# Kernel tuning notes

Measured on AMD Instinct MI355X. Metric: run time of the kernel, lower is better.

The kernel has to match this reference:

```python
import jax, jax.numpy as jnp
import numpy as np

MODEL_DIM = 1024
N_HEADS = 16
HEAD_DIM = 64  # q_dim == k_dim == v_dim


def setup_inputs() -> dict:
    key = jax.random.key(0)
    ks = jax.random.split(key, 7)
    B, S = 4, 2048
    scale = 1.0 / np.sqrt(MODEL_DIM)
    return {
        "q": jax.random.normal(ks[0], (B, S, MODEL_DIM), dtype=jnp.float32),
        "k": jax.random.normal(ks[1], (B, S, MODEL_DIM), dtype=jnp.float32),
        "v": jax.random.normal(ks[2], (B, S, MODEL_DIM), dtype=jnp.float32),
        # Linear weights stored as [out, in] like torch; no biases.
        "wq": jax.random.normal(ks[3], (N_HEADS * HEAD_DIM, MODEL_DIM), dtype=jnp.float32) * scale,
        "wk": jax.random.normal(ks[4], (N_HEADS * HEAD_DIM, MODEL_DIM), dtype=jnp.float32) * scale,
        "wv": jax.random.normal(ks[5], (N_HEADS * HEAD_DIM, MODEL_DIM), dtype=jnp.float32) * scale,
        "wo": jax.random.normal(ks[6], (MODEL_DIM, N_HEADS * HEAD_DIM), dtype=jnp.float32) * scale,
    }


def reference(q, k, v, wq, wk, wv, wo):
    B, Sq, _ = q.shape
    Sk = k.shape[1]
    # projections: [B,S,D] @ W^T -> [B,S,H*dh] -> [B,H,S,dh]
    qh = (q @ wq.T).reshape(B, Sq, N_HEADS, HEAD_DIM).transpose(0, 2, 1, 3)
    kh = (k @ wk.T).reshape(B, Sk, N_HEADS, HEAD_DIM).transpose(0, 2, 1, 3)
    vh = (v @ wv.T).reshape(B, Sk, N_HEADS, HEAD_DIM).transpose(0, 2, 1, 3)
    # scores [B,H,Sq,Sk], scaled by sqrt(k_dim)
    scores = jnp.einsum('bhqd,bhkd->bhqk', qh, kh) / jnp.sqrt(jnp.float32(HEAD_DIM))
    attn = jax.nn.softmax(scores, axis=-1)
    ctx = jnp.einsum('bhqk,bhkd->bhqd', attn, vh)  # [B,H,Sq,dh]
    ctx = ctx.transpose(0, 2, 1, 3).reshape(B, Sq, N_HEADS * HEAD_DIM)
    return ctx @ wo.T
```

## Files before the change

### kernel.cpp

```cpp
#include <hip/hip_runtime.h>
#include <cstdint>
#include <cstddef>


typedef _Float16 f16x8 __attribute__((ext_vector_type(8)));
typedef _Float16 f16x4 __attribute__((ext_vector_type(4)));
typedef _Float16 f16x2 __attribute__((ext_vector_type(2)));
typedef __fp16 h16x2 __attribute__((ext_vector_type(2)));
typedef float f32x4 __attribute__((ext_vector_type(4)));
typedef float f32x16 __attribute__((ext_vector_type(16)));
typedef unsigned u32x4 __attribute__((ext_vector_type(4)));
typedef int i32x2 __attribute__((ext_vector_type(2)));

#define LDS_CAST(p) ((__attribute__((address_space(3))) void*)(p))
#define GLB_CAST(p) ((const __attribute__((address_space(1))) void*)(p))

__device__ __forceinline__ void gload_lds16(const void* g, void* l) {
  __builtin_amdgcn_global_load_lds(GLB_CAST(g), LDS_CAST(l), 16, 0, 0);
}

__device__ __forceinline__ float fexp2(float x) {
#if __has_builtin(__builtin_amdgcn_exp2f)
  return __builtin_amdgcn_exp2f(x);
#else
  return exp2f(x);
#endif
}

__device__ __forceinline__ f16x2 pkrtz(float a, float b) {
  h16x2 r = __builtin_amdgcn_cvt_pkrtz(a, b);
  return __builtin_bit_cast(f16x2, r);
}

__device__ __forceinline__ float dot2acc(f16x2 a, float acc) {
#if __has_builtin(__builtin_amdgcn_fdot2)
  const f16x2 one2 = {(_Float16)1.0f, (_Float16)1.0f};
  return __builtin_amdgcn_fdot2(a, one2, acc, false);
#else
  return acc + (float)a[0] + (float)a[1];
#endif
}

__device__ __forceinline__ void pl32swap(unsigned& a, unsigned& b) {
#if __has_builtin(__builtin_amdgcn_permlane32_swap)
  i32x2 r = __builtin_amdgcn_permlane32_swap((int)a, (int)b, false, false);
  a = (unsigned)r[0];
  b = (unsigned)r[1];
#else
  asm("v_permlane32_swap_b32 %0, %1" : "+v"(a), "+v"(b));
#endif
}

__global__ void cvt3_kernel(const float* __restrict__ a,
                            const float* __restrict__ b,
                            const float* __restrict__ c,
                            _Float16* __restrict__ oa, _Float16* __restrict__ ob,
                            _Float16* __restrict__ oc) {
  const float* in = blockIdx.z == 0 ? a : blockIdx.z == 1 ? b : c;
  _Float16* out = blockIdx.z == 0 ? oa : blockIdx.z == 1 ? ob : oc;
  int i = blockIdx.x * 256 + threadIdx.x;
  float4 v = ((const float4*)in)[i];
  f16x4 o = {(_Float16)v.x, (_Float16)v.y, (_Float16)v.z, (_Float16)v.w};
  ((f16x4*)out)[i] = o;
}

__global__ void cvt4_kernel(const float* __restrict__ a,
                            const float* __restrict__ b,
                            const float* __restrict__ c,
                            const float* __restrict__ d,
                            _Float16* __restrict__ oa, _Float16* __restrict__ ob,
                            _Float16* __restrict__ oc, _Float16* __restrict__ od) {
  int z = blockIdx.z;
  const float* in = z == 0 ? a : z == 1 ? b : z == 2 ? c : d;
  _Float16* out = z == 0 ? oa : z == 1 ? ob : z == 2 ? oc : od;
  int i = blockIdx.x * 256 + threadIdx.x;
  float4 v = ((const float4*)in)[i];
  f16x4 o = {(_Float16)v.x, (_Float16)v.y, (_Float16)v.z, (_Float16)v.w};
  ((f16x4*)out)[i] = o;
}

template <int MODE>
__device__ __forceinline__ void gemm_core(const _Float16* __restrict__ A,
                                          const _Float16* __restrict__ W,
                                          void* __restrict__ C, float scale,
                                          _Float16* As, _Float16* Bs) {
  constexpr int K = 1024, N = 1024;
  const int tid = threadIdx.x;
  const int wid = tid >> 6;
  const int lane = tid & 63;
  const int quad = lane >> 4;
  const int l16 = lane & 15;
  const int wm = wid >> 1;
  const int wn = wid & 1;
  const int m0 = blockIdx.y * 128;
  const int n0 = blockIdx.x * 128;

  const _Float16* Ag = A + (size_t)m0 * K;
  const _Float16* Bg = W + (size_t)n0 * K;

  f32x4 acc[4][4];
#pragma unroll
  for (int i = 0; i < 4; i++)
#pragma unroll
    for (int j = 0; j < 4; j++) acc[i][j] = (f32x4){0.f, 0.f, 0.f, 0.f};

  const int lrow = lane >> 2;
  const int lcol = (lane & 3) * 8;

  for (int k0 = 0; k0 < K; k0 += 32) {
#pragma unroll
    for (int i = 0; i < 2; i++) {
      int issue = wid * 2 + i;
      gload_lds16(Ag + (size_t)(issue * 16 + lrow) * K + k0 + lcol,
                  &As[issue * 512]);
      gload_lds16(Bg + (size_t)(issue * 16 + lrow) * K + k0 + lcol,
                  &Bs[issue * 512]);
    }
    __syncthreads();
    f16x8 af[4], bfr[4];
#pragma unroll
    for (int mt = 0; mt < 4; mt++)
      af[mt] = *(const f16x8*)&As[(wm * 64 + mt * 16 + l16) * 32 + quad * 8];
#pragma unroll
    for (int nt = 0; nt < 4; nt++)
      bfr[nt] = *(const f16x8*)&Bs[(wn * 64 + nt * 16 + l16) * 32 + quad * 8];
#pragma unroll
    for (int mt = 0; mt < 4; mt++)
#pragma unroll
      for (int nt = 0; nt < 4; nt++)
        acc[mt][nt] = __builtin_amdgcn_mfma_f32_16x16x32_f16(
            af[mt], bfr[nt], acc[mt][nt], 0, 0, 0);
    __syncthreads();
  }

#pragma unroll
  for (int mt = 0; mt < 4; mt++) {
#pragma unroll
    for (int nt = 0; nt < 4; nt++) {
#pragma unroll
      for (int r = 0; r < 4; r++) {
        int m = m0 + wm * 64 + mt * 16 + quad * 4 + r;
        int n = n0 + wn * 64 + nt * 16 + l16;
        float v = acc[mt][nt][r] * scale;
        if (MODE == 0) {
          ((float*)C)[(size_t)m * N + n] = v;
        } else {
          int b = m >> 11, s = m & 2047;
          int h = n >> 6, dd = n & 63;
          size_t bh = (size_t)(b * 16 + h);
          if (MODE == 1) {
            ((_Float16*)C)[(bh * 2048 + s) * 64 + dd] = (_Float16)v;
          } else if (MODE == 3) {
            int kt2 = s >> 5, l32k = s & 31;
            int s4 = dd >> 4, hi8 = (dd >> 3) & 1, j = dd & 7;
            size_t idx =
                ((((bh * 64 + kt2) * 4 + s4) * 2 + hi8) * 32 + l32k) * 8 + j;
            ((_Float16*)C)[idx] = (_Float16)v;
          } else {
            int kt = s >> 6, ks = (s >> 4) & 3, hi8 = (s >> 3) & 1, j = s & 7;
            int dt = dd >> 5, l32v = dd & 31;
            size_t idx =
                ((((bh * 32 + kt) * 2 + dt) * 4 + ks) * 64 + hi8 * 32 + l32v) *
                    8 +
                j;
            ((_Float16*)C)[idx] = (_Float16)v;
          }
        }
      }
    }
  }
}

__global__ __launch_bounds__(256) void gemm_qkv(
    const _Float16* __restrict__ qb, const _Float16* __restrict__ kb,
    const _Float16* __restrict__ vb, const _Float16* __restrict__ wq,
    const _Float16* __restrict__ wk, const _Float16* __restrict__ wv,
    _Float16* __restrict__ Qh, _Float16* __restrict__ Kf,
    _Float16* __restrict__ Vf) {
  __shared__ _Float16 As[128 * 32];
  __shared__ _Float16 Bs[128 * 32];
  if (blockIdx.z == 0)
    gemm_core<1>(qb, wq, Qh, 0.18033688f, As, Bs);
  else if (blockIdx.z == 1)
    gemm_core<3>(kb, wk, Kf, 1.0f, As, Bs);
  else
    gemm_core<4>(vb, wv, Vf, 1.0f, As, Bs);
}

__global__ __launch_bounds__(256) void gemm_wo(const _Float16* __restrict__ ctx,
                                               const _Float16* __restrict__ wo,
                                               float* __restrict__ out) {
  __shared__ _Float16 As[128 * 32];
  __shared__ _Float16 Bs[128 * 32];
  gemm_core<0>(ctx, wo, out, 1.0f, As, Bs);
}

__global__ __launch_bounds__(256, 4) void attn_kernel(
    const _Float16* __restrict__ Qh, const _Float16* __restrict__ Kf,
    const _Float16* __restrict__ Vf, _Float16* __restrict__ ctx) {
  const int qt = blockIdx.x;
  const int bh = blockIdx.y;
  const int tid = threadIdx.x;
  const int wid = tid >> 6;
  const int lane = tid & 63;
  const int l32 = lane & 31;
  const int hi = lane >> 5;

  const _Float16* Qg = Qh + ((size_t)bh * 2048 + qt * 128 + wid * 32) * 64;
  const _Float16* Kb = Kf + (size_t)bh * 131072;
  const _Float16* Vb = Vf + (size_t)bh * 131072;

  f16x8 aq[4];
#pragma unroll
  for (int s = 0; s < 4; s++)
    aq[s] = *(const f16x8*)(Qg + (size_t)l32 * 64 + s * 16 + hi * 8);

  f32x16 acc[2];
#pragma unroll
  for (int i = 0; i < 16; i++) {
    acc[0][i] = 0.f;
    acc[1][i] = 0.f;
  }
  float lsA = 0.f, lsB = 0.f;

  for (int kt = 0; kt < 32; kt++) {
    const _Float16* Kt = Kb + kt * 4096;
    const _Float16* Vt = Vb + kt * 4096;

    f16x8 kf[2][4];
#pragma unroll
    for (int st = 0; st < 2; st++)
#pragma unroll
      for (int s = 0; s < 4; s++)
        kf[st][s] = *(const f16x8*)(Kt + ((st * 4 + s) * 64 + lane) * 8);

    unsigned hw[2][8];
    {
      f32x16 sacc;
#pragma unroll
      for (int i = 0; i < 16; i++) sacc[i] = 0.f;
#pragma unroll
      for (int s = 0; s < 4; s++)
        sacc =
            __builtin_amdgcn_mfma_f32_32x32x16_f16(kf[0][s], aq[s], sacc, 0, 0, 0);

      f16x8 vf0[4], vf1[4];
#pragma unroll
      for (int g = 0; g < 4; g++) {
        vf0[g] = *(const f16x8*)(Vt + ((0 * 4 + g) * 64 + lane) * 8);
        vf1[g] = *(const f16x8*)(Vt + ((1 * 4 + g) * 64 + lane) * 8);
      }

#pragma unroll
      for (int i = 0; i < 8; i++) {
        float p0 = fexp2(sacc[2 * i]);
        float p1 = fexp2(sacc[2 * i + 1]);
        f16x2 hh = pkrtz(p0, p1);
        if (i & 1)
          lsB = dot2acc(hh, lsB);
        else
          lsA = dot2acc(hh, lsA);
        hw[0][i] = __builtin_bit_cast(unsigned, hh);
      }

      f32x16 sacc1;
#pragma unroll
      for (int i = 0; i < 16; i++) sacc1[i] = 0.f;
#pragma unroll
      for (int s = 0; s < 4; s++)
        sacc1 = __builtin_amdgcn_mfma_f32_32x32x16_f16(kf[1][s], aq[s], sacc1,
                                                       0, 0, 0);
#pragma unroll
      for (int i = 0; i < 8; i++) {
        float p0 = fexp2(sacc1[2 * i]);
        float p1 = fexp2(sacc1[2 * i + 1]);
        f16x2 hh = pkrtz(p0, p1);
        if (i & 1)
          lsB = dot2acc(hh, lsB);
        else
          lsA = dot2acc(hh, lsA);
        hw[1][i] = __builtin_bit_cast(unsigned, hh);
      }

#pragma unroll
      for (int st = 0; st < 2; st++)
#pragma unroll
        for (int kh = 0; kh < 2; kh++) {
          unsigned w0 = hw[st][4 * kh + 0], w2 = hw[st][4 * kh + 2];
          unsigned w1 = hw[st][4 * kh + 1], w3 = hw[st][4 * kh + 3];
          pl32swap(w0, w2);
          pl32swap(w1, w3);
          u32x4 wv = {w0, w1, w2, w3};
          f16x8 pfrag = __builtin_bit_cast(f16x8, wv);
          int g = st * 2 + kh;
          acc[0] = __builtin_amdgcn_mfma_f32_32x32x16_f16(vf0[g], pfrag, acc[0],
                                                          0, 0, 0);
          acc[1] = __builtin_amdgcn_mfma_f32_32x32x16_f16(vf1[g], pfrag, acc[1],
                                                          0, 0, 0);
        }
    }
  }

  float lsum = lsA + lsB;
  float l = lsum + __shfl_xor(lsum, 32);
  float inv = 1.f / l;
  const int b = bh >> 4, h = bh & 15;
  int q = qt * 128 + wid * 32 + l32;
  _Float16* outp = ctx + ((size_t)b * 2048 + q) * 1024 + h * 64;
#pragma unroll
  for (int dt = 0; dt < 2; dt++)
#pragma unroll
    for (int g = 0; g < 4; g++) {
      f16x4 o;
#pragma unroll
      for (int c = 0; c < 4; c++) o[c] = (_Float16)(acc[dt][g * 4 + c] * inv);
      *(f16x4*)(outp + dt * 32 + g * 8 + hi * 4) = o;
    }
}

extern "C" void kernel_launch(void* const* d_in, const int* in_sizes, int n_in,
                              void* d_out, int out_size, void* d_ws,
                              size_t ws_size, hipStream_t stream) {
  const float* q = (const float*)d_in[0];
  const float* k = (const float*)d_in[1];
  const float* v = (const float*)d_in[2];
  const float* wq = (const float*)d_in[3];
  const float* wk = (const float*)d_in[4];
  const float* wv = (const float*)d_in[5];
  const float* wo = (const float*)d_in[6];
  float* out = (float*)d_out;

  const size_t SD = (size_t)8192 * 1024;
  const size_t WSZ = (size_t)1024 * 1024;

  _Float16* ws = (_Float16*)d_ws;
  _Float16* qb = ws;
  _Float16* kb = ws + 1 * SD;
  _Float16* vb = ws + 2 * SD;
  _Float16* Qh = ws + 3 * SD;
  _Float16* Kf = ws + 4 * SD;
  _Float16* Vf = ws + 5 * SD;
  _Float16* ctx = ws + 6 * SD;
  _Float16* wqb = ws + 7 * SD;
  _Float16* wkb = wqb + WSZ;
  _Float16* wvb = wqb + 2 * WSZ;
  _Float16* wob = wqb + 3 * WSZ;

  cvt3_kernel<<<dim3(8192, 1, 3), 256, 0, stream>>>(q, k, v, qb, kb, vb);
  cvt4_kernel<<<dim3(1024, 1, 4), 256, 0, stream>>>(wq, wk, wv, wo, wqb, wkb,
                                                    wvb, wob);

  gemm_qkv<<<dim3(8, 64, 3), 256, 0, stream>>>(qb, kb, vb, wqb, wkb, wvb, Qh,
                                               Kf, Vf);

  attn_kernel<<<dim3(16, 64), 256, 0, stream>>>(Qh, Kf, Vf, ctx);

  gemm_wo<<<dim3(8, 64), 256, 0, stream>>>(ctx, wob, out);
}
```

Baseline: 350.8 us.

## Interleave K/V tiles and stage them through triple-buffered LDS in attention

The K and V projection outputs are written into one interleaved buffer so that each 64-key tile of K and V is contiguous. The attention kernel then prefetches the next K/V tile into LDS with direct global-to-LDS loads, using a three-slot ring buffer and a barrier, instead of every wave reading K/V straight from global memory. This is meant to share K/V loads across the four waves of a block and hide load latency behind the MFMA work. In exchange it adds 48KB of LDS per block, lowers the occupancy bound from 4 to 3 blocks, and adds a barrier every iteration.

New measurement: 334.6 us. 4.6% less time.

```diff
diff --git a/kernel.cpp b/kernel.cpp
--- a/kernel.cpp
+++ b/kernel.cpp
@@ -153,16 +153,15 @@
           } else if (MODE == 3) {
             int kt2 = s >> 5, l32k = s & 31;
             int s4 = dd >> 4, hi8 = (dd >> 3) & 1, j = dd & 7;
-            size_t idx =
-                ((((bh * 64 + kt2) * 4 + s4) * 2 + hi8) * 32 + l32k) * 8 + j;
+            size_t idx = (bh * 32 + (kt2 >> 1)) * 8192 +
+                         (((kt2 & 1) * 4 + s4) * 512) + (hi8 * 32 + l32k) * 8 +
+                         j;
             ((_Float16*)C)[idx] = (_Float16)v;
           } else {
             int kt = s >> 6, ks = (s >> 4) & 3, hi8 = (s >> 3) & 1, j = s & 7;
             int dt = dd >> 5, l32v = dd & 31;
-            size_t idx =
-                ((((bh * 32 + kt) * 2 + dt) * 4 + ks) * 64 + hi8 * 32 + l32v) *
-                    8 +
-                j;
+            size_t idx = (bh * 32 + kt) * 8192 + 4096 + ((dt * 4 + ks) * 512) +
+                         (hi8 * 32 + l32v) * 8 + j;
             ((_Float16*)C)[idx] = (_Float16)v;
           }
         }
@@ -175,16 +174,15 @@
     const _Float16* __restrict__ qb, const _Float16* __restrict__ kb,
     const _Float16* __restrict__ vb, const _Float16* __restrict__ wq,
     const _Float16* __restrict__ wk, const _Float16* __restrict__ wv,
-    _Float16* __restrict__ Qh, _Float16* __restrict__ Kf,
-    _Float16* __restrict__ Vf) {
+    _Float16* __restrict__ Qh, _Float16* __restrict__ KVf) {
   __shared__ _Float16 As[128 * 32];
   __shared__ _Float16 Bs[128 * 32];
   if (blockIdx.z == 0)
     gemm_core<1>(qb, wq, Qh, 0.18033688f, As, Bs);
   else if (blockIdx.z == 1)
-    gemm_core<3>(kb, wk, Kf, 1.0f, As, Bs);
+    gemm_core<3>(kb, wk, KVf, 1.0f, As, Bs);
   else
-    gemm_core<4>(vb, wv, Vf, 1.0f, As, Bs);
+    gemm_core<4>(vb, wv, KVf, 1.0f, As, Bs);
 }
 
 __global__ __launch_bounds__(256) void gemm_wo(const _Float16* __restrict__ ctx,
@@ -195,9 +193,11 @@
   gemm_core<0>(ctx, wo, out, 1.0f, As, Bs);
 }
 
-__global__ __launch_bounds__(256, 4) void attn_kernel(
-    const _Float16* __restrict__ Qh, const _Float16* __restrict__ Kf,
-    const _Float16* __restrict__ Vf, _Float16* __restrict__ ctx) {
+__global__ __launch_bounds__(256, 3) void attn_kernel(
+    const _Float16* __restrict__ Qh, const _Float16* __restrict__ KVf,
+    _Float16* __restrict__ ctx) {
+  __shared__ _Float16 sKV[3][8192];
+
   const int qt = blockIdx.x;
   const int bh = blockIdx.y;
   const int tid = threadIdx.x;
@@ -207,8 +207,7 @@
   const int hi = lane >> 5;
 
   const _Float16* Qg = Qh + ((size_t)bh * 2048 + qt * 128 + wid * 32) * 64;
-  const _Float16* Kb = Kf + (size_t)bh * 131072;
-  const _Float16* Vb = Vf + (size_t)bh * 131072;
+  const _Float16* KVb = KVf + (size_t)bh * 262144;
 
   f16x8 aq[4];
 #pragma unroll
@@ -223,82 +222,96 @@
   }
   float lsA = 0.f, lsB = 0.f;
 
+  auto stage = [&](int buf, int kt) {
+    const _Float16* t = KVb + (size_t)kt * 8192;
+#pragma unroll
+    for (int i = 0; i < 4; i++) {
+      int c = wid * 4 + i;
+      gload_lds16(t + c * 512 + lane * 8, &sKV[buf][c * 512]);
+    }
+  };
+
+  stage(0, 0);
+  int cur = 0;
+
   for (int kt = 0; kt < 32; kt++) {
-    const _Float16* Kt = Kb + kt * 4096;
-    const _Float16* Vt = Vb + kt * 4096;
-
-    f16x8 kf[2][4];
+    int nxt = (cur == 2) ? 0 : cur + 1;
+    if (kt < 31) {
+      stage(nxt, kt + 1);
+      asm volatile("s_waitcnt vmcnt(4)" ::: "memory");
+    } else {
+      asm volatile("s_waitcnt vmcnt(0)" ::: "memory");
+    }
+    __builtin_amdgcn_s_barrier();
+    asm volatile("" ::: "memory");
+
+    const _Float16* Ks = sKV[cur];
+    const _Float16* Vs = sKV[cur] + 4096;
+
+    f16x8 kf0[4], kf1[4];
+#pragma unroll
+    for (int s = 0; s < 4; s++) {
+      kf0[s] = *(const f16x8*)&Ks[(0 * 4 + s) * 512 + lane * 8];
+      kf1[s] = *(const f16x8*)&Ks[(4 + s) * 512 + lane * 8];
+    }
+
+    f32x16 s0, s1;
+#pragma unroll
+    for (int i = 0; i < 16; i++) {
+      s0[i] = 0.f;
+      s1[i] = 0.f;
+    }
+#pragma unroll
+    for (int s = 0; s < 4; s++) {
+      s0 = __builtin_amdgcn_mfma_f32_32x32x16_f16(kf0[s], aq[s], s0, 0, 0, 0);
+      s1 = __builtin_amdgcn_mfma_f32_32x32x16_f16(kf1[s], aq[s], s1, 0, 0, 0);
+    }
+
+    f16x8 vf0[4], vf1[4];
+#pragma unroll
+    for (int g = 0; g < 4; g++) {
+      vf0[g] = *(const f16x8*)&Vs[(0 * 4 + g) * 512 + lane * 8];
+      vf1[g] = *(const f16x8*)&Vs[(4 + g) * 512 + lane * 8];
+    }
+
+    unsigned hw[2][8];
+#pragma unroll
+    for (int i = 0; i < 8; i++) {
+      f16x2 hh = pkrtz(fexp2(s0[2 * i]), fexp2(s0[2 * i + 1]));
+      if (i & 1)
+        lsB = dot2acc(hh, lsB);
+      else
+        lsA = dot2acc(hh, lsA);
+      hw[0][i] = __builtin_bit_cast(unsigned, hh);
+    }
+#pragma unroll
+    for (int i = 0; i < 8; i++) {
+      f16x2 hh = pkrtz(fexp2(s1[2 * i]), fexp2(s1[2 * i + 1]));
+      if (i & 1)
+        lsB = dot2acc(hh, lsB);
+      else
+        lsA = dot2acc(hh, lsA);
+      hw[1][i] = __builtin_bit_cast(unsigned, hh);
+    }
+
 #pragma unroll
     for (int st = 0; st < 2; st++)
 #pragma unroll
-      for (int s = 0; s < 4; s++)
-        kf[st][s] = *(const f16x8*)(Kt + ((st * 4 + s) * 64 + lane) * 8);
-
-    unsigned hw[2][8];
-    {
-      f32x16 sacc;
-#pragma unroll
-      for (int i = 0; i < 16; i++) sacc[i] = 0.f;
-#pragma unroll
-      for (int s = 0; s < 4; s++)
-        sacc =
-            __builtin_amdgcn_mfma_f32_32x32x16_f16(kf[0][s], aq[s], sacc, 0, 0, 0);
-
-      f16x8 vf0[4], vf1[4];
-#pragma unroll
-      for (int g = 0; g < 4; g++) {
-        vf0[g] = *(const f16x8*)(Vt + ((0 * 4 + g) * 64 + lane) * 8);
-        vf1[g] = *(const f16x8*)(Vt + ((1 * 4 + g) * 64 + lane) * 8);
+      for (int kh = 0; kh < 2; kh++) {
+        unsigned w0 = hw[st][4 * kh + 0], w2 = hw[st][4 * kh + 2];
+        unsigned w1 = hw[st][4 * kh + 1], w3 = hw[st][4 * kh + 3];
+        pl32swap(w0, w2);
+        pl32swap(w1, w3);
+        u32x4 wv4 = {w0, w1, w2, w3};
+        f16x8 pfrag = __builtin_bit_cast(f16x8, wv4);
+        int g = st * 2 + kh;
+        acc[0] = __builtin_amdgcn_mfma_f32_32x32x16_f16(vf0[g], pfrag, acc[0],
+                                                        0, 0, 0);
+        acc[1] = __builtin_amdgcn_mfma_f32_32x32x16_f16(vf1[g], pfrag, acc[1],
+                                                        0, 0, 0);
       }
 
-#pragma unroll
-      for (int i = 0; i < 8; i++) {
-        float p0 = fexp2(sacc[2 * i]);
-        float p1 = fexp2(sacc[2 * i + 1]);
-        f16x2 hh = pkrtz(p0, p1);
-        if (i & 1)
-          lsB = dot2acc(hh, lsB);
-        else
-          lsA = dot2acc(hh, lsA);
-        hw[0][i] = __builtin_bit_cast(unsigned, hh);
-      }
-
-      f32x16 sacc1;
-#pragma unroll
-      for (int i = 0; i < 16; i++) sacc1[i] = 0.f;
-#pragma unroll
-      for (int s = 0; s < 4; s++)
-        sacc1 = __builtin_amdgcn_mfma_f32_32x32x16_f16(kf[1][s], aq[s], sacc1,
-                                                       0, 0, 0);
-#pragma unroll
-      for (int i = 0; i < 8; i++) {
-        float p0 = fexp2(sacc1[2 * i]);
-        float p1 = fexp2(sacc1[2 * i + 1]);
-        f16x2 hh = pkrtz(p0, p1);
-        if (i & 1)
-          lsB = dot2acc(hh, lsB);
-        else
-          lsA = dot2acc(hh, lsA);
-        hw[1][i] = __builtin_bit_cast(unsigned, hh);
-      }
-
-#pragma unroll
-      for (int st = 0; st < 2; st++)
-#pragma unroll
-        for (int kh = 0; kh < 2; kh++) {
-          unsigned w0 = hw[st][4 * kh + 0], w2 = hw[st][4 * kh + 2];
-          unsigned w1 = hw[st][4 * kh + 1], w3 = hw[st][4 * kh + 3];
-          pl32swap(w0, w2);
-          pl32swap(w1, w3);
-          u32x4 wv = {w0, w1, w2, w3};
-          f16x8 pfrag = __builtin_bit_cast(f16x8, wv);
-          int g = st * 2 + kh;
-          acc[0] = __builtin_amdgcn_mfma_f32_32x32x16_f16(vf0[g], pfrag, acc[0],
-                                                          0, 0, 0);
-          acc[1] = __builtin_amdgcn_mfma_f32_32x32x16_f16(vf1[g], pfrag, acc[1],
-                                                          0, 0, 0);
-        }
-    }
+    cur = nxt;
   }
 
   float lsum = lsA + lsB;
@@ -338,8 +351,7 @@
   _Float16* kb = ws + 1 * SD;
   _Float16* vb = ws + 2 * SD;
   _Float16* Qh = ws + 3 * SD;
-  _Float16* Kf = ws + 4 * SD;
-  _Float16* Vf = ws + 5 * SD;
+  _Float16* KVf = ws + 4 * SD;
   _Float16* ctx = ws + 6 * SD;
   _Float16* wqb = ws + 7 * SD;
   _Float16* wkb = wqb + WSZ;
@@ -351,9 +363,9 @@
                                                     wvb, wob);
 
   gemm_qkv<<<dim3(8, 64, 3), 256, 0, stream>>>(qb, kb, vb, wqb, wkb, wvb, Qh,
-                                               Kf, Vf);
-
-  attn_kernel<<<dim3(16, 64), 256, 0, stream>>>(Qh, Kf, Vf, ctx);
+                                               KVf);
+
+  attn_kernel<<<dim3(16, 64), 256, 0, stream>>>(Qh, KVf, ctx);
 
   gemm_wo<<<dim3(8, 64), 256, 0, stream>>>(ctx, wob, out);
 }
```
